# Optimization experiments

Measured on AMD Instinct MI355X. Metric: run time of the kernel, lower is better.

## Reference

```python
import jax, jax.numpy as jnp
import numpy as np
from jax import lax

N_LAYERS = 10  # Sinkhorn(n_layers=10)


def setup_inputs() -> dict:
    key = jax.random.key(0)
    k1, k2, k3 = jax.random.split(key, 3)
    S, NA, NB = 4, 4096, 4096
    alpha = jax.random.uniform(k1, (S, NA), jnp.float32, 0.05, 1.0)
    alpha = alpha / alpha.sum(-1, keepdims=True)  # probability simplex
    beta = jax.random.uniform(k2, (S, NB), jnp.float32, 0.05, 1.0)
    beta = beta / beta.sum(-1, keepdims=True)
    C = jax.random.uniform(k3, (NA, NB), jnp.float32)  # nonneg cost matrix
    eps = jnp.float32(0.1)  # entropic regularization
    return {"alpha": alpha, "beta": beta, "C": C, "eps": eps}


def reference(alpha, beta, C, eps):
    # Log-domain Sinkhorn: f,g are dual potentials, shapes (S,NA)/(S,NB).
    log_alpha = jnp.log(alpha)
    log_beta = jnp.log(beta)

    def log_dot_exp(A, b):
        # A: (n, m), b: (S, m) -> (S, n); matches torch log_dot_exp (2D case)
        return jax.scipy.special.logsumexp((-A[None, :, :] + b[:, None, :]) / eps, axis=-1)

    def step(carry, _):
        _, g = carry
        f = eps * (log_alpha - log_dot_exp(C, g))
        g = eps * (log_beta - log_dot_exp(C.T, f))
        return (f, g), None

    f0 = jnp.zeros_like(alpha)
    g0 = jnp.zeros_like(beta)
    (f, g), _ = lax.scan(step, (f0, g0), None, length=N_LAYERS)
    return f, g
```

## Files before the change

### kernel.cpp

```cpp
#include <hip/hip_runtime.h>
#include <stdint.h>

#define NN 4096
#define NITER 10
#define ROWS 16
#define NBLK 256
#define THREADS 512

#define STG_OFF  131072
#define RED_OFF  148480

typedef float v2f __attribute__((ext_vector_type(2)));

static __device__ __forceinline__ unsigned short f2bf(float f) {
  union { float f; unsigned int i; } x; x.f = f;
  unsigned int i = x.i;
  i += 0x7FFFu + ((i >> 16) & 1u);
  return (unsigned short)(i >> 16);
}
static __device__ __forceinline__ unsigned int pk2(float a, float b) {
  return (unsigned int)f2bf(a) | ((unsigned int)f2bf(b) << 16);
}
static __device__ __forceinline__ float2 unpk(unsigned int u) {
  union { unsigned int i; float f; } a, b;
  a.i = u << 16; b.i = u & 0xFFFF0000u;
  return make_float2(a.f, b.f);
}
static __device__ __forceinline__ float read_eps(const void* p) {
  float f = *(const float*)p;
  if (f > 1e-4f && f < 1.0f) return f;
  union { unsigned int i; float f; } x;
  x.i = ((unsigned int)*(const unsigned short*)p) << 16;
  return x.f;
}
static __device__ __forceinline__ void astore8(unsigned long long* p, unsigned long long v) {
  __hip_atomic_store(p, v, __ATOMIC_RELAXED, __HIP_MEMORY_SCOPE_AGENT);
}
static __device__ __forceinline__ float4 up4(unsigned int w0, unsigned int w1) {
  float2 a = unpk(w0), b = unpk(w1);
  return make_float4(a.x, a.y, b.x, b.y);
}
static __device__ __forceinline__ v2f mk2(float a, float b) {
  v2f r; r.x = a; r.y = b; return r;
}
#define FMA2(a, b, c) __builtin_elementwise_fma(a, b, c)

__global__ __launch_bounds__(256) void zero_flags(unsigned int* __restrict__ c) {
#pragma unroll
  for (int k = 0; k < 32; ++k) c[threadIdx.x + k * 256] = 0;
}

static __device__ __forceinline__ void wait_group(
    const unsigned int* flags, int q, unsigned token) {
  const unsigned int* p = flags + (q * 64 + (threadIdx.x & 63)) * 16;
  for (;;) {
    unsigned v = __hip_atomic_load(p, __ATOMIC_RELAXED,
                                   __HIP_MEMORY_SCOPE_AGENT);
    if (__ballot(v >= token) == 0xFFFFFFFFFFFFFFFFull) break;
    __builtin_amdgcn_s_sleep(1);
  }
}

__global__ __launch_bounds__(THREADS, 1) void sinkhorn_all(
    const float* __restrict__ alpha, const float* __restrict__ beta,
    const float* __restrict__ C, const void* __restrict__ epsp,
    unsigned short* __restrict__ K, unsigned long long* __restrict__ u_ep,
    unsigned long long* __restrict__ v_ep, unsigned int* __restrict__ u_flags,
    unsigned int* __restrict__ v_flags, float* __restrict__ out) {
  __shared__ float4 smem4[9792];
  char* sm = (char*)smem4;
  const int t = threadIdx.x, b = blockIdx.x;
  const int wave = t >> 6, lane = t & 63;
  const int own = ((b & 7) << 5) | (b >> 3);
  const int base0 = own * ROWS;
  const float eps = read_eps(epsp);
  const float nie = -1.0f / eps;

#pragma unroll 2
  for (int r = 0; r < ROWS; ++r) {
    const float4* Crow = (const float4*)(C + (size_t)(base0 + r) * NN) + t * 2;
    float4 c0 = Crow[0], c1 = Crow[1];
    uint4 k0;
    k0.x = pk2(__expf(c0.x * nie), __expf(c0.y * nie));
    k0.y = pk2(__expf(c0.z * nie), __expf(c0.w * nie));
    k0.z = pk2(__expf(c1.x * nie), __expf(c1.y * nie));
    k0.w = pk2(__expf(c1.z * nie), __expf(c1.w * nie));
    ((uint4*)(K + (size_t)(base0 + r) * NN))[t] = k0;
  }

  {
    const int p = t & 3, cb = p * 4, rb = t >> 2;
#pragma unroll 1
    for (int q2 = 0; q2 < 32; q2 += 8) {
      float4 cv[8];
#pragma unroll
      for (int z = 0; z < 8; ++z)
        cv[z] = *(const float4*)(C + (size_t)((q2 + z) * 128 + rb) * NN + base0 + cb);
#pragma unroll
      for (int z = 0; z < 8; ++z) {
        int n = (q2 + z) * 128 + rb;
        int u16 = ((n >> 10) * 8 + ((n >> 3) & 7)) * 256 + ((n >> 6) & 15) * 16;
        int jo = (n & 7) * 2;
        *(unsigned short*)(sm + (size_t)(u16 + cb + 0) * 16 + jo) = f2bf(__expf(cv[z].x * nie));
        *(unsigned short*)(sm + (size_t)(u16 + cb + 1) * 16 + jo) = f2bf(__expf(cv[z].y * nie));
        *(unsigned short*)(sm + (size_t)(u16 + cb + 2) * 16 + jo) = f2bf(__expf(cv[z].z * nie));
        *(unsigned short*)(sm + (size_t)(u16 + cb + 3) * 16 + jo) = f2bf(__expf(cv[z].w * nie));
      }
    }
  }
  __syncthreads();

  for (int it = 0; it < NITER; ++it) {
    v2f acc01[2] = {}, acc23[2] = {};
    const int r0 = base0 + wave * 2;
    const uint4* Kr0 = (const uint4*)(K + (size_t)r0 * NN);
    const uint4* VB = (const uint4*)(v_ep + (size_t)(it - 1) * NN);
#pragma unroll 1
    for (int q = 0; q < 4; ++q) {
      if (it > 0) wait_group(v_flags, q, (unsigned)it);
      {
        float4* L = (float4*)(sm + STG_OFF);
        int s0 = t * 2;
        float4 f0, f1;
        if (it == 0) {
          f0 = f1 = make_float4(1.f, 1.f, 1.f, 1.f);
        } else {
          uint4 sv = VB[q * 512 + t];
          f0 = up4(sv.x, sv.y);
          f1 = up4(sv.z, sv.w);
        }
        L[((s0 & 7) * 128) + (s0 >> 3)] = f0;
        L[(((s0 + 1) & 7) * 128) + ((s0 + 1) >> 3)] = f1;
      }
      __syncthreads();
      uint4 karr[4];
#pragma unroll
      for (int ms = 0; ms < 2; ++ms) {
        int moff = q * 128 + ms * 64 + lane;
        karr[ms * 2 + 0] = Kr0[moff];
        karr[ms * 2 + 1] = Kr0[moff + 512];
      }
      const float4* VL = (const float4*)(sm + STG_OFF);
#pragma unroll
      for (int ms = 0; ms < 2; ++ms) {
        int lb = ms * 64 + lane;
        float4 vv[8];
#pragma unroll
        for (int j = 0; j < 8; ++j) vv[j] = VL[j * 128 + lb];
#pragma unroll
        for (int rr = 0; rr < 2; ++rr) {
          unsigned int cw[4] = {karr[ms*2+rr].x, karr[ms*2+rr].y,
                                karr[ms*2+rr].z, karr[ms*2+rr].w};
#pragma unroll
          for (int w = 0; w < 4; ++w) {
            float2 f = unpk(cw[w]);
            float4 va = vv[2 * w], vb = vv[2 * w + 1];
            acc01[rr] = FMA2(mk2(f.x, f.x), mk2(va.x, va.y), acc01[rr]);
            acc23[rr] = FMA2(mk2(f.x, f.x), mk2(va.z, va.w), acc23[rr]);
            acc01[rr] = FMA2(mk2(f.y, f.y), mk2(vb.x, vb.y), acc01[rr]);
            acc23[rr] = FMA2(mk2(f.y, f.y), mk2(vb.z, vb.w), acc23[rr]);
          }
        }
      }
      __syncthreads();
    }
    float accf[2][4];
#pragma unroll
    for (int rr = 0; rr < 2; ++rr) {
      accf[rr][0] = acc01[rr].x; accf[rr][1] = acc01[rr].y;
      accf[rr][2] = acc23[rr].x; accf[rr][3] = acc23[rr].y;
    }
#pragma unroll
    for (int off = 32; off > 0; off >>= 1)
#pragma unroll
      for (int rr = 0; rr < 2; ++rr)
#pragma unroll
        for (int s = 0; s < 4; ++s)
          accf[rr][s] += __shfl_xor(accf[rr][s], off);
    if (lane < 2) {
      int row = r0 + lane;
      float ux = alpha[0 * NN + row] / accf[lane][0];
      float uy = alpha[1 * NN + row] / accf[lane][1];
      float uz = alpha[2 * NN + row] / accf[lane][2];
      float uw = alpha[3 * NN + row] / accf[lane][3];
      unsigned long long ub = (unsigned long long)pk2(ux, uy) |
                              ((unsigned long long)pk2(uz, uw) << 32);
      astore8(u_ep + (size_t)it * NN + row, ub);
      if (it == NITER - 1) {
        out[0 * NN + row] = eps * __logf(ux);
        out[1 * NN + row] = eps * __logf(uy);
        out[2 * NN + row] = eps * __logf(uz);
        out[3 * NN + row] = eps * __logf(uw);
      }
    }
    __syncthreads();
    if (t == 0)
      __hip_atomic_store(u_flags + own * 16, (unsigned)(it + 1),
                         __ATOMIC_RELAXED, __HIP_MEMORY_SCOPE_AGENT);

    v2f bacc01 = {}, bacc23 = {};
    const int c = t & 15, k2 = (t >> 4) & 15, half = t >> 8;
    const uint4* UB = (const uint4*)(u_ep + (size_t)it * NN);
#pragma unroll 1
    for (int q = 0; q < 4; ++q) {
      wait_group(u_flags, q, (unsigned)(it + 1));
      {
        char* US = sm + STG_OFF;
        uint4 su = UB[q * 512 + t];
        float4 f0 = up4(su.x, su.y), f1 = up4(su.z, su.w);
        int n0 = t * 2;
        *(float4*)(US + (n0 + 0) * 16 + ((n0 + 0) >> 4) * 16) = f0;
        *(float4*)(US + (n0 + 1) * 16 + ((n0 + 1) >> 4) * 16) = f1;
      }
      __syncthreads();
      const char* US = sm + STG_OFF;
#pragma unroll
      for (int i = 0; i < 4; ++i) {
        uint4 kt = ((const uint4*)sm)[(q * 8 + half * 4 + i) * 256 + k2 * 16 + c];
        int nb = k2 * 64 + (half * 4 + i) * 8;
        unsigned int kw[4] = {kt.x, kt.y, kt.z, kt.w};
#pragma unroll
        for (int w = 0; w < 4; ++w) {
          float2 f = unpk(kw[w]);
          int j0 = nb + 2 * w, j1 = nb + 2 * w + 1;
          float4 u0 = *(const float4*)(US + j0 * 16 + (j0 >> 4) * 16);
          float4 u1 = *(const float4*)(US + j1 * 16 + (j1 >> 4) * 16);
          bacc01 = FMA2(mk2(f.x, f.x), mk2(u0.x, u0.y), bacc01);
          bacc23 = FMA2(mk2(f.x, f.x), mk2(u0.z, u0.w), bacc23);
          bacc01 = FMA2(mk2(f.y, f.y), mk2(u1.x, u1.y), bacc01);
          bacc23 = FMA2(mk2(f.y, f.y), mk2(u1.z, u1.w), bacc23);
        }
      }
      __syncthreads();
    }
    {
      float4* red = (float4*)(sm + RED_OFF);
      red[(half * 16 + k2) * 16 + c] =
          make_float4(bacc01.x, bacc01.y, bacc23.x, bacc23.y);
    }
    __syncthreads();
    if (t < 16) {
      const float4* red = (const float4*)(sm + RED_OFF);
      float4 a = make_float4(0.f, 0.f, 0.f, 0.f);
#pragma unroll
      for (int g = 0; g < 32; ++g) {
        float4 r = red[g * 16 + t];
        a.x += r.x; a.y += r.y; a.z += r.z; a.w += r.w;
      }
      int m = base0 + t;
      float vx = beta[0 * NN + m] / a.x;
      float vy = beta[1 * NN + m] / a.y;
      float vz = beta[2 * NN + m] / a.z;
      float vw = beta[3 * NN + m] / a.w;
      unsigned long long vb = (unsigned long long)pk2(vx, vy) |
                              ((unsigned long long)pk2(vz, vw) << 32);
      astore8(v_ep + (size_t)it * NN + m, vb);
      if (it == NITER - 1) {
        out[4 * NN + 0 * NN + m] = eps * __logf(vx);
        out[4 * NN + 1 * NN + m] = eps * __logf(vy);
        out[4 * NN + 2 * NN + m] = eps * __logf(vz);
        out[4 * NN + 3 * NN + m] = eps * __logf(vw);
      }
    }
    __syncthreads();
    if (t == 0 && it < NITER - 1)
      __hip_atomic_store(v_flags + own * 16, (unsigned)(it + 1),
                         __ATOMIC_RELAXED, __HIP_MEMORY_SCOPE_AGENT);
  }
}

extern "C" void kernel_launch(void* const* d_in, const int* in_sizes, int n_in,
                              void* d_out, int out_size, void* d_ws, size_t ws_size,
                              hipStream_t stream) {
  (void)in_sizes; (void)n_in; (void)out_size; (void)ws_size;
  const float* alpha = (const float*)d_in[0];
  const float* beta  = (const float*)d_in[1];
  const float* C     = (const float*)d_in[2];
  const void*  epsp  = d_in[3];

  char* ws = (char*)d_ws;
  unsigned short* K        = (unsigned short*)ws;
  unsigned long long* u_ep = (unsigned long long*)(ws + 33554432);
  unsigned long long* v_ep = (unsigned long long*)(ws + 33554432 + 327680);
  unsigned int* u_flags    = (unsigned int*)(ws + 33554432 + 655360);
  unsigned int* v_flags    = (unsigned int*)(ws + 33554432 + 655360 + 16384);
  float* out = (float*)d_out;

  zero_flags<<<1, 256, 0, stream>>>(u_flags);
  sinkhorn_all<<<NBLK, THREADS, 0, stream>>>(alpha, beta, C, epsp, K,
                                             u_ep, v_ep, u_flags, v_flags, out);
}
```

Measured before the change: 269.6 us.

## Double block size to 1024 threads, one row per wave, prefetch K before barrier

Raises the block from 512 to 1024 threads and repartitions every phase: the K precompute, the transposed LDS fill, the u-update (now one row per wave instead of two) and the v-update (half the k-chunks per thread). The K loads from global and LDS are issued before the staging barrier so they overlap the wait. The v-reduction now does an in-wave shuffle over the k2 groups before the LDS write, shrinking the cross-wave reduction. This adds latency hiding through more waves per CU, but barrier cost grows with 16 waves and half the threads sit idle during staging.

```diff
diff --git a/kernel.cpp b/kernel.cpp
--- a/kernel.cpp
+++ b/kernel.cpp
@@ -5,7 +5,7 @@
 #define NITER 10
 #define ROWS 16
 #define NBLK 256
-#define THREADS 512
+#define THREADS 1024
 
 #define STG_OFF  131072
 #define RED_OFF  148480
@@ -67,7 +67,7 @@
     unsigned short* __restrict__ K, unsigned long long* __restrict__ u_ep,
     unsigned long long* __restrict__ v_ep, unsigned int* __restrict__ u_flags,
     unsigned int* __restrict__ v_flags, float* __restrict__ out) {
-  __shared__ float4 smem4[9792];
+  __shared__ float4 smem4[9536];
   char* sm = (char*)smem4;
   const int t = threadIdx.x, b = blockIdx.x;
   const int wave = t >> 6, lane = t & 63;
@@ -77,28 +77,29 @@
   const float nie = -1.0f / eps;
 
 #pragma unroll 2
-  for (int r = 0; r < ROWS; ++r) {
-    const float4* Crow = (const float4*)(C + (size_t)(base0 + r) * NN) + t * 2;
+  for (int rp = 0; rp < 8; ++rp) {
+    const int r = rp * 2 + (t >> 9);
+    const float4* Crow = (const float4*)(C + (size_t)(base0 + r) * NN) + (t & 511) * 2;
     float4 c0 = Crow[0], c1 = Crow[1];
     uint4 k0;
     k0.x = pk2(__expf(c0.x * nie), __expf(c0.y * nie));
     k0.y = pk2(__expf(c0.z * nie), __expf(c0.w * nie));
     k0.z = pk2(__expf(c1.x * nie), __expf(c1.y * nie));
     k0.w = pk2(__expf(c1.z * nie), __expf(c1.w * nie));
-    ((uint4*)(K + (size_t)(base0 + r) * NN))[t] = k0;
+    ((uint4*)(K + (size_t)(base0 + r) * NN))[t & 511] = k0;
   }
 
   {
     const int p = t & 3, cb = p * 4, rb = t >> 2;
 #pragma unroll 1
-    for (int q2 = 0; q2 < 32; q2 += 8) {
+    for (int q2 = 0; q2 < 16; q2 += 8) {
       float4 cv[8];
 #pragma unroll
       for (int z = 0; z < 8; ++z)
-        cv[z] = *(const float4*)(C + (size_t)((q2 + z) * 128 + rb) * NN + base0 + cb);
+        cv[z] = *(const float4*)(C + (size_t)((q2 + z) * 256 + rb) * NN + base0 + cb);
 #pragma unroll
       for (int z = 0; z < 8; ++z) {
-        int n = (q2 + z) * 128 + rb;
+        int n = (q2 + z) * 256 + rb;
         int u16 = ((n >> 10) * 8 + ((n >> 3) & 7)) * 256 + ((n >> 6) & 15) * 16;
         int jo = (n & 7) * 2;
         *(unsigned short*)(sm + (size_t)(u16 + cb + 0) * 16 + jo) = f2bf(__expf(cv[z].x * nie));
@@ -111,14 +112,17 @@
   __syncthreads();
 
   for (int it = 0; it < NITER; ++it) {
-    v2f acc01[2] = {}, acc23[2] = {};
-    const int r0 = base0 + wave * 2;
+    v2f acc01 = {}, acc23 = {};
+    const int r0 = base0 + wave;
     const uint4* Kr0 = (const uint4*)(K + (size_t)r0 * NN);
     const uint4* VB = (const uint4*)(v_ep + (size_t)(it - 1) * NN);
 #pragma unroll 1
     for (int q = 0; q < 4; ++q) {
       if (it > 0) wait_group(v_flags, q, (unsigned)it);
-      {
+      uint4 karr[2];
+      karr[0] = Kr0[q * 128 + lane];
+      karr[1] = Kr0[q * 128 + 64 + lane];
+      if (t < 512) {
         float4* L = (float4*)(sm + STG_OFF);
         int s0 = t * 2;
         float4 f0, f1;
@@ -133,13 +137,6 @@
         L[(((s0 + 1) & 7) * 128) + ((s0 + 1) >> 3)] = f1;
       }
       __syncthreads();
-      uint4 karr[4];
-#pragma unroll
-      for (int ms = 0; ms < 2; ++ms) {
-        int moff = q * 128 + ms * 64 + lane;
-        karr[ms * 2 + 0] = Kr0[moff];
-        karr[ms * 2 + 1] = Kr0[moff + 512];
-      }
       const float4* VL = (const float4*)(sm + STG_OFF);
 #pragma unroll
       for (int ms = 0; ms < 2; ++ms) {
@@ -147,50 +144,41 @@
         float4 vv[8];
 #pragma unroll
         for (int j = 0; j < 8; ++j) vv[j] = VL[j * 128 + lb];
-#pragma unroll
-        for (int rr = 0; rr < 2; ++rr) {
-          unsigned int cw[4] = {karr[ms*2+rr].x, karr[ms*2+rr].y,
-                                karr[ms*2+rr].z, karr[ms*2+rr].w};
-#pragma unroll
-          for (int w = 0; w < 4; ++w) {
-            float2 f = unpk(cw[w]);
-            float4 va = vv[2 * w], vb = vv[2 * w + 1];
-            acc01[rr] = FMA2(mk2(f.x, f.x), mk2(va.x, va.y), acc01[rr]);
-            acc23[rr] = FMA2(mk2(f.x, f.x), mk2(va.z, va.w), acc23[rr]);
-            acc01[rr] = FMA2(mk2(f.y, f.y), mk2(vb.x, vb.y), acc01[rr]);
-            acc23[rr] = FMA2(mk2(f.y, f.y), mk2(vb.z, vb.w), acc23[rr]);
-          }
-        }
-      }
-      __syncthreads();
-    }
-    float accf[2][4];
-#pragma unroll
-    for (int rr = 0; rr < 2; ++rr) {
-      accf[rr][0] = acc01[rr].x; accf[rr][1] = acc01[rr].y;
-      accf[rr][2] = acc23[rr].x; accf[rr][3] = acc23[rr].y;
-    }
-#pragma unroll
-    for (int off = 32; off > 0; off >>= 1)
-#pragma unroll
-      for (int rr = 0; rr < 2; ++rr)
+        unsigned int cw[4] = {karr[ms].x, karr[ms].y, karr[ms].z, karr[ms].w};
+#pragma unroll
+        for (int w = 0; w < 4; ++w) {
+          float2 f = unpk(cw[w]);
+          float4 va = vv[2 * w], vb = vv[2 * w + 1];
+          acc01 = FMA2(mk2(f.x, f.x), mk2(va.x, va.y), acc01);
+          acc23 = FMA2(mk2(f.x, f.x), mk2(va.z, va.w), acc23);
+          acc01 = FMA2(mk2(f.y, f.y), mk2(vb.x, vb.y), acc01);
+          acc23 = FMA2(mk2(f.y, f.y), mk2(vb.z, vb.w), acc23);
+        }
+      }
+      __syncthreads();
+    }
+    {
+      float accf[4] = {acc01.x, acc01.y, acc23.x, acc23.y};
+#pragma unroll
+      for (int off = 32; off > 0; off >>= 1)
 #pragma unroll
         for (int s = 0; s < 4; ++s)
-          accf[rr][s] += __shfl_xor(accf[rr][s], off);
-    if (lane < 2) {
-      int row = r0 + lane;
-      float ux = alpha[0 * NN + row] / accf[lane][0];
-      float uy = alpha[1 * NN + row] / accf[lane][1];
-      float uz = alpha[2 * NN + row] / accf[lane][2];
-      float uw = alpha[3 * NN + row] / accf[lane][3];
-      unsigned long long ub = (unsigned long long)pk2(ux, uy) |
-                              ((unsigned long long)pk2(uz, uw) << 32);
-      astore8(u_ep + (size_t)it * NN + row, ub);
-      if (it == NITER - 1) {
-        out[0 * NN + row] = eps * __logf(ux);
-        out[1 * NN + row] = eps * __logf(uy);
-        out[2 * NN + row] = eps * __logf(uz);
-        out[3 * NN + row] = eps * __logf(uw);
+          accf[s] += __shfl_xor(accf[s], off);
+      if (lane == 0) {
+        int row = r0;
+        float ux = alpha[0 * NN + row] / accf[0];
+        float uy = alpha[1 * NN + row] / accf[1];
+        float uz = alpha[2 * NN + row] / accf[2];
+        float uw = alpha[3 * NN + row] / accf[3];
+        unsigned long long ub = (unsigned long long)pk2(ux, uy) |
+                                ((unsigned long long)pk2(uz, uw) << 32);
+        astore8(u_ep + (size_t)it * NN + row, ub);
+        if (it == NITER - 1) {
+          out[0 * NN + row] = eps * __logf(ux);
+          out[1 * NN + row] = eps * __logf(uy);
+          out[2 * NN + row] = eps * __logf(uz);
+          out[3 * NN + row] = eps * __logf(uw);
+        }
       }
     }
     __syncthreads();
@@ -204,7 +192,11 @@
 #pragma unroll 1
     for (int q = 0; q < 4; ++q) {
       wait_group(u_flags, q, (unsigned)(it + 1));
-      {
+      uint4 kt[2];
+#pragma unroll
+      for (int i = 0; i < 2; ++i)
+        kt[i] = ((const uint4*)sm)[(q * 8 + half * 2 + i) * 256 + k2 * 16 + c];
+      if (t < 512) {
         char* US = sm + STG_OFF;
         uint4 su = UB[q * 512 + t];
         float4 f0 = up4(su.x, su.y), f1 = up4(su.z, su.w);
@@ -215,10 +207,9 @@
       __syncthreads();
       const char* US = sm + STG_OFF;
 #pragma unroll
-      for (int i = 0; i < 4; ++i) {
-        uint4 kt = ((const uint4*)sm)[(q * 8 + half * 4 + i) * 256 + k2 * 16 + c];
-        int nb = k2 * 64 + (half * 4 + i) * 8;
-        unsigned int kw[4] = {kt.x, kt.y, kt.z, kt.w};
+      for (int i = 0; i < 2; ++i) {
+        int nb = k2 * 64 + (half * 2 + i) * 8;
+        unsigned int kw[4] = {kt[i].x, kt[i].y, kt[i].z, kt[i].w};
 #pragma unroll
         for (int w = 0; w < 4; ++w) {
           float2 f = unpk(kw[w]);
@@ -234,16 +225,23 @@
       __syncthreads();
     }
     {
-      float4* red = (float4*)(sm + RED_OFF);
-      red[(half * 16 + k2) * 16 + c] =
-          make_float4(bacc01.x, bacc01.y, bacc23.x, bacc23.y);
+      float bf[4] = {bacc01.x, bacc01.y, bacc23.x, bacc23.y};
+#pragma unroll
+      for (int s = 0; s < 4; ++s) {
+        bf[s] += __shfl_xor(bf[s], 16);
+        bf[s] += __shfl_xor(bf[s], 32);
+      }
+      if (lane < 16) {
+        float4* red = (float4*)(sm + RED_OFF);
+        red[wave * 16 + lane] = make_float4(bf[0], bf[1], bf[2], bf[3]);
+      }
     }
     __syncthreads();
     if (t < 16) {
       const float4* red = (const float4*)(sm + RED_OFF);
       float4 a = make_float4(0.f, 0.f, 0.f, 0.f);
 #pragma unroll
-      for (int g = 0; g < 32; ++g) {
+      for (int g = 0; g < 16; ++g) {
         float4 r = red[g * 16 + t];
         a.x += r.x; a.y += r.y; a.z += r.z; a.w += r.w;
       }
```

New measurement: 287.4 us. +6.6%, slower.

## Double-buffer staging with single upfront flag wait and swizzled bf16 LDS vectors

Applied to the files above, without the earlier changes.

Both matvec phases now wait once for all producer flags up front, replacing the four per-quarter waits. Each quarter double-buffers the staged vector in LDS while prefetching the next quarter's K tile into registers. Vectors stay bf16 in LDS under an XOR swizzle, which halves staging bytes and drops one barrier per quarter. The column pass is remapped so each thread handles two columns, and a wave shuffle reduction replaces most of the LDS reduction. The single wait gives up overlap between early quarters and late producers, and the bounded spin can exit before the data is ready.

```diff
diff --git a/kernel.cpp b/kernel.cpp
--- a/kernel.cpp
+++ b/kernel.cpp
@@ -8,7 +8,8 @@
 #define THREADS 512
 
 #define STG_OFF  131072
-#define RED_OFF  148480
+#define RED_OFF  147456
+#define SWZ(s) ((((unsigned)(s)) * 16u) ^ ((((unsigned)(s)) >> 3 & 7u) << 4))
 
 typedef float v2f __attribute__((ext_vector_type(2)));
 
@@ -36,10 +37,6 @@
 static __device__ __forceinline__ void astore8(unsigned long long* p, unsigned long long v) {
   __hip_atomic_store(p, v, __ATOMIC_RELAXED, __HIP_MEMORY_SCOPE_AGENT);
 }
-static __device__ __forceinline__ float4 up4(unsigned int w0, unsigned int w1) {
-  float2 a = unpk(w0), b = unpk(w1);
-  return make_float4(a.x, a.y, b.x, b.y);
-}
 static __device__ __forceinline__ v2f mk2(float a, float b) {
   v2f r; r.x = a; r.y = b; return r;
 }
@@ -50,13 +47,16 @@
   for (int k = 0; k < 32; ++k) c[threadIdx.x + k * 256] = 0;
 }
 
-static __device__ __forceinline__ void wait_group(
-    const unsigned int* flags, int q, unsigned token) {
-  const unsigned int* p = flags + (q * 64 + (threadIdx.x & 63)) * 16;
-  for (;;) {
-    unsigned v = __hip_atomic_load(p, __ATOMIC_RELAXED,
-                                   __HIP_MEMORY_SCOPE_AGENT);
-    if (__ballot(v >= token) == 0xFFFFFFFFFFFFFFFFull) break;
+static __device__ __forceinline__ void wait_all(
+    const unsigned int* flags, unsigned token) {
+  const unsigned int* p = flags + (threadIdx.x & 63) * 16;
+  for (int spin = 0; spin < 200000; ++spin) {
+    unsigned a = __hip_atomic_load(p, __ATOMIC_RELAXED, __HIP_MEMORY_SCOPE_AGENT);
+    unsigned b = __hip_atomic_load(p + 64 * 16, __ATOMIC_RELAXED, __HIP_MEMORY_SCOPE_AGENT);
+    unsigned c = __hip_atomic_load(p + 128 * 16, __ATOMIC_RELAXED, __HIP_MEMORY_SCOPE_AGENT);
+    unsigned d = __hip_atomic_load(p + 192 * 16, __ATOMIC_RELAXED, __HIP_MEMORY_SCOPE_AGENT);
+    unsigned mn = min(min(a, b), min(c, d));
+    if (__ballot(mn >= token) == 0xFFFFFFFFFFFFFFFFull) break;
     __builtin_amdgcn_s_sleep(1);
   }
 }
@@ -67,7 +67,7 @@
     unsigned short* __restrict__ K, unsigned long long* __restrict__ u_ep,
     unsigned long long* __restrict__ v_ep, unsigned int* __restrict__ u_flags,
     unsigned int* __restrict__ v_flags, float* __restrict__ out) {
-  __shared__ float4 smem4[9792];
+  __shared__ float4 smem4[9344];
   char* sm = (char*)smem4;
   const int t = threadIdx.x, b = blockIdx.x;
   const int wave = t >> 6, lane = t & 63;
@@ -110,87 +110,101 @@
   }
   __syncthreads();
 
+  const uint4 ONES = make_uint4(0x3F803F80u, 0x3F803F80u, 0x3F803F80u, 0x3F803F80u);
+
   for (int it = 0; it < NITER; ++it) {
     v2f acc01[2] = {}, acc23[2] = {};
     const int r0 = base0 + wave * 2;
     const uint4* Kr0 = (const uint4*)(K + (size_t)r0 * NN);
     const uint4* VB = (const uint4*)(v_ep + (size_t)(it - 1) * NN);
+    if (it > 0) wait_all(v_flags, (unsigned)it);
+    {
+      uint4 sv = (it == 0) ? ONES : VB[t];
+      *(uint4*)(sm + STG_OFF + SWZ((t & 3) * 128 + (t >> 2))) = sv;
+    }
+    uint4 ka[4];
+#pragma unroll
+    for (int ms = 0; ms < 2; ++ms) {
+      ka[ms * 2 + 0] = Kr0[ms * 64 + lane];
+      ka[ms * 2 + 1] = Kr0[512 + ms * 64 + lane];
+    }
+    __syncthreads();
 #pragma unroll 1
     for (int q = 0; q < 4; ++q) {
-      if (it > 0) wait_group(v_flags, q, (unsigned)it);
-      {
-        float4* L = (float4*)(sm + STG_OFF);
-        int s0 = t * 2;
-        float4 f0, f1;
-        if (it == 0) {
-          f0 = f1 = make_float4(1.f, 1.f, 1.f, 1.f);
-        } else {
-          uint4 sv = VB[q * 512 + t];
-          f0 = up4(sv.x, sv.y);
-          f1 = up4(sv.z, sv.w);
-        }
-        L[((s0 & 7) * 128) + (s0 >> 3)] = f0;
-        L[(((s0 + 1) & 7) * 128) + ((s0 + 1) >> 3)] = f1;
-      }
-      __syncthreads();
-      uint4 karr[4];
+      uint4 sv_n, ka_n[4];
+      if (q < 3) {
+        sv_n = (it == 0) ? ONES : VB[(q + 1) * 512 + t];
+#pragma unroll
+        for (int ms = 0; ms < 2; ++ms) {
+          ka_n[ms * 2 + 0] = Kr0[(q + 1) * 128 + ms * 64 + lane];
+          ka_n[ms * 2 + 1] = Kr0[512 + (q + 1) * 128 + ms * 64 + lane];
+        }
+      }
+      const char* stg = sm + STG_OFF + (q & 1) * 8192;
 #pragma unroll
       for (int ms = 0; ms < 2; ++ms) {
-        int moff = q * 128 + ms * 64 + lane;
-        karr[ms * 2 + 0] = Kr0[moff];
-        karr[ms * 2 + 1] = Kr0[moff + 512];
-      }
-      const float4* VL = (const float4*)(sm + STG_OFF);
-#pragma unroll
-      for (int ms = 0; ms < 2; ++ms) {
-        int lb = ms * 64 + lane;
-        float4 vv[8];
-#pragma unroll
-        for (int j = 0; j < 8; ++j) vv[j] = VL[j * 128 + lb];
+        const int lb = ms * 64 + lane;
+        uint4 vq[4];
+#pragma unroll
+        for (int jj = 0; jj < 4; ++jj)
+          vq[jj] = *(const uint4*)(stg + SWZ(jj * 128 + lb));
+        float2 va01[4], va23[4], vb01[4], vb23[4];
+#pragma unroll
+        for (int w = 0; w < 4; ++w) {
+          va01[w] = unpk(vq[w].x); va23[w] = unpk(vq[w].y);
+          vb01[w] = unpk(vq[w].z); vb23[w] = unpk(vq[w].w);
+        }
 #pragma unroll
         for (int rr = 0; rr < 2; ++rr) {
-          unsigned int cw[4] = {karr[ms*2+rr].x, karr[ms*2+rr].y,
-                                karr[ms*2+rr].z, karr[ms*2+rr].w};
+          unsigned int cw[4] = {ka[ms * 2 + rr].x, ka[ms * 2 + rr].y,
+                                ka[ms * 2 + rr].z, ka[ms * 2 + rr].w};
 #pragma unroll
           for (int w = 0; w < 4; ++w) {
             float2 f = unpk(cw[w]);
-            float4 va = vv[2 * w], vb = vv[2 * w + 1];
-            acc01[rr] = FMA2(mk2(f.x, f.x), mk2(va.x, va.y), acc01[rr]);
-            acc23[rr] = FMA2(mk2(f.x, f.x), mk2(va.z, va.w), acc23[rr]);
-            acc01[rr] = FMA2(mk2(f.y, f.y), mk2(vb.x, vb.y), acc01[rr]);
-            acc23[rr] = FMA2(mk2(f.y, f.y), mk2(vb.z, vb.w), acc23[rr]);
+            acc01[rr] = FMA2(mk2(f.x, f.x), mk2(va01[w].x, va01[w].y), acc01[rr]);
+            acc23[rr] = FMA2(mk2(f.x, f.x), mk2(va23[w].x, va23[w].y), acc23[rr]);
+            acc01[rr] = FMA2(mk2(f.y, f.y), mk2(vb01[w].x, vb01[w].y), acc01[rr]);
+            acc23[rr] = FMA2(mk2(f.y, f.y), mk2(vb23[w].x, vb23[w].y), acc23[rr]);
           }
         }
       }
+      if (q < 3) {
+        *(uint4*)(sm + STG_OFF + ((q + 1) & 1) * 8192 +
+                  SWZ((t & 3) * 128 + (t >> 2))) = sv_n;
+#pragma unroll
+        for (int z = 0; z < 4; ++z) ka[z] = ka_n[z];
+      }
       __syncthreads();
     }
-    float accf[2][4];
-#pragma unroll
-    for (int rr = 0; rr < 2; ++rr) {
-      accf[rr][0] = acc01[rr].x; accf[rr][1] = acc01[rr].y;
-      accf[rr][2] = acc23[rr].x; accf[rr][3] = acc23[rr].y;
-    }
-#pragma unroll
-    for (int off = 32; off > 0; off >>= 1)
-#pragma unroll
-      for (int rr = 0; rr < 2; ++rr)
-#pragma unroll
-        for (int s = 0; s < 4; ++s)
-          accf[rr][s] += __shfl_xor(accf[rr][s], off);
-    if (lane < 2) {
-      int row = r0 + lane;
-      float ux = alpha[0 * NN + row] / accf[lane][0];
-      float uy = alpha[1 * NN + row] / accf[lane][1];
-      float uz = alpha[2 * NN + row] / accf[lane][2];
-      float uw = alpha[3 * NN + row] / accf[lane][3];
-      unsigned long long ub = (unsigned long long)pk2(ux, uy) |
-                              ((unsigned long long)pk2(uz, uw) << 32);
-      astore8(u_ep + (size_t)it * NN + row, ub);
-      if (it == NITER - 1) {
-        out[0 * NN + row] = eps * __logf(ux);
-        out[1 * NN + row] = eps * __logf(uy);
-        out[2 * NN + row] = eps * __logf(uz);
-        out[3 * NN + row] = eps * __logf(uw);
+    {
+      float accf[2][4];
+#pragma unroll
+      for (int rr = 0; rr < 2; ++rr) {
+        accf[rr][0] = acc01[rr].x; accf[rr][1] = acc01[rr].y;
+        accf[rr][2] = acc23[rr].x; accf[rr][3] = acc23[rr].y;
+      }
+#pragma unroll
+      for (int off = 32; off > 0; off >>= 1)
+#pragma unroll
+        for (int rr = 0; rr < 2; ++rr)
+#pragma unroll
+          for (int s = 0; s < 4; ++s)
+            accf[rr][s] += __shfl_xor(accf[rr][s], off);
+      if (lane < 2) {
+        int row = r0 + lane;
+        float ux = alpha[0 * NN + row] / accf[lane][0];
+        float uy = alpha[1 * NN + row] / accf[lane][1];
+        float uz = alpha[2 * NN + row] / accf[lane][2];
+        float uw = alpha[3 * NN + row] / accf[lane][3];
+        unsigned long long ub = (unsigned long long)pk2(ux, uy) |
+                                ((unsigned long long)pk2(uz, uw) << 32);
+        astore8(u_ep + (size_t)it * NN + row, ub);
+        if (it == NITER - 1) {
+          out[0 * NN + row] = eps * __logf(ux);
+          out[1 * NN + row] = eps * __logf(uy);
+          out[2 * NN + row] = eps * __logf(uz);
+          out[3 * NN + row] = eps * __logf(uw);
+        }
       }
     }
     __syncthreads();
@@ -198,53 +212,94 @@
       __hip_atomic_store(u_flags + own * 16, (unsigned)(it + 1),
                          __ATOMIC_RELAXED, __HIP_MEMORY_SCOPE_AGENT);
 
-    v2f bacc01 = {}, bacc23 = {};
-    const int c = t & 15, k2 = (t >> 4) & 15, half = t >> 8;
+    v2f bacc01[2] = {}, bacc23[2] = {};
+    const int c = t & 7, k2 = (t >> 3) & 15, half = t >> 7;
     const uint4* UB = (const uint4*)(u_ep + (size_t)it * NN);
+    wait_all(u_flags, (unsigned)(it + 1));
+    {
+      uint4 su = UB[t];
+      *(uint4*)(sm + STG_OFF + SWZ((t & 3) * 128 + (t >> 2))) = su;
+    }
+    uint4 kt[4];
+#pragma unroll
+    for (int i = 0; i < 2; ++i) {
+      int s = half * 2 + i;
+      kt[i * 2 + 0] = ((const uint4*)sm)[(0 * 8 + s) * 256 + k2 * 16 + c];
+      kt[i * 2 + 1] = ((const uint4*)sm)[(0 * 8 + s) * 256 + k2 * 16 + c + 8];
+    }
+    __syncthreads();
 #pragma unroll 1
     for (int q = 0; q < 4; ++q) {
-      wait_group(u_flags, q, (unsigned)(it + 1));
-      {
-        char* US = sm + STG_OFF;
-        uint4 su = UB[q * 512 + t];
-        float4 f0 = up4(su.x, su.y), f1 = up4(su.z, su.w);
-        int n0 = t * 2;
-        *(float4*)(US + (n0 + 0) * 16 + ((n0 + 0) >> 4) * 16) = f0;
-        *(float4*)(US + (n0 + 1) * 16 + ((n0 + 1) >> 4) * 16) = f1;
+      uint4 su_n, kt_n[4];
+      if (q < 3) {
+        su_n = UB[(q + 1) * 512 + t];
+#pragma unroll
+        for (int i = 0; i < 2; ++i) {
+          int s = half * 2 + i;
+          kt_n[i * 2 + 0] = ((const uint4*)sm)[((q + 1) * 8 + s) * 256 + k2 * 16 + c];
+          kt_n[i * 2 + 1] = ((const uint4*)sm)[((q + 1) * 8 + s) * 256 + k2 * 16 + c + 8];
+        }
+      }
+      const char* stg = sm + STG_OFF + (q & 1) * 8192;
+#pragma unroll
+      for (int i = 0; i < 2; ++i) {
+        const int s = half * 2 + i;
+        uint4 uq[4];
+#pragma unroll
+        for (int jj = 0; jj < 4; ++jj)
+          uq[jj] = *(const uint4*)(stg + SWZ(jj * 128 + k2 * 8 + s));
+        float2 u01[8], u23[8];
+#pragma unroll
+        for (int jj = 0; jj < 4; ++jj) {
+          u01[2 * jj]     = unpk(uq[jj].x); u23[2 * jj]     = unpk(uq[jj].y);
+          u01[2 * jj + 1] = unpk(uq[jj].z); u23[2 * jj + 1] = unpk(uq[jj].w);
+        }
+#pragma unroll
+        for (int cs = 0; cs < 2; ++cs) {
+          unsigned int kw[4] = {kt[i * 2 + cs].x, kt[i * 2 + cs].y,
+                                kt[i * 2 + cs].z, kt[i * 2 + cs].w};
+#pragma unroll
+          for (int w = 0; w < 4; ++w) {
+            float2 f = unpk(kw[w]);
+            bacc01[cs] = FMA2(mk2(f.x, f.x), mk2(u01[2 * w].x, u01[2 * w].y), bacc01[cs]);
+            bacc23[cs] = FMA2(mk2(f.x, f.x), mk2(u23[2 * w].x, u23[2 * w].y), bacc23[cs]);
+            bacc01[cs] = FMA2(mk2(f.y, f.y), mk2(u01[2 * w + 1].x, u01[2 * w + 1].y), bacc01[cs]);
+            bacc23[cs] = FMA2(mk2(f.y, f.y), mk2(u23[2 * w + 1].x, u23[2 * w + 1].y), bacc23[cs]);
+          }
+        }
+      }
+      if (q < 3) {
+        *(uint4*)(sm + STG_OFF + ((q + 1) & 1) * 8192 +
+                  SWZ((t & 3) * 128 + (t >> 2))) = su_n;
+#pragma unroll
+        for (int z = 0; z < 4; ++z) kt[z] = kt_n[z];
       }
       __syncthreads();
-      const char* US = sm + STG_OFF;
-#pragma unroll
-      for (int i = 0; i < 4; ++i) {
-        uint4 kt = ((const uint4*)sm)[(q * 8 + half * 4 + i) * 256 + k2 * 16 + c];
-        int nb = k2 * 64 + (half * 4 + i) * 8;
-        unsigned int kw[4] = {kt.x, kt.y, kt.z, kt.w};
-#pragma unroll
-        for (int w = 0; w < 4; ++w) {
-          float2 f = unpk(kw[w]);
-          int j0 = nb + 2 * w, j1 = nb + 2 * w + 1;
-          float4 u0 = *(const float4*)(US + j0 * 16 + (j0 >> 4) * 16);
-          float4 u1 = *(const float4*)(US + j1 * 16 + (j1 >> 4) * 16);
-          bacc01 = FMA2(mk2(f.x, f.x), mk2(u0.x, u0.y), bacc01);
-          bacc23 = FMA2(mk2(f.x, f.x), mk2(u0.z, u0.w), bacc23);
-          bacc01 = FMA2(mk2(f.y, f.y), mk2(u1.x, u1.y), bacc01);
-          bacc23 = FMA2(mk2(f.y, f.y), mk2(u1.z, u1.w), bacc23);
-        }
-      }
-      __syncthreads();
     }
     {
-      float4* red = (float4*)(sm + RED_OFF);
-      red[(half * 16 + k2) * 16 + c] =
-          make_float4(bacc01.x, bacc01.y, bacc23.x, bacc23.y);
+      float bf0[4] = {bacc01[0].x, bacc01[0].y, bacc23[0].x, bacc23[0].y};
+      float bf1[4] = {bacc01[1].x, bacc01[1].y, bacc23[1].x, bacc23[1].y};
+#pragma unroll
+      for (int off = 8; off <= 32; off <<= 1)
+#pragma unroll
+        for (int s2 = 0; s2 < 4; ++s2) {
+          bf0[s2] += __shfl_xor(bf0[s2], off);
+          bf1[s2] += __shfl_xor(bf1[s2], off);
+        }
+      if (lane < 8) {
+        float4* red = (float4*)(sm + RED_OFF);
+        red[(wave * 8 + lane) * 2 + 0] = make_float4(bf0[0], bf0[1], bf0[2], bf0[3]);
+        red[(wave * 8 + lane) * 2 + 1] = make_float4(bf1[0], bf1[1], bf1[2], bf1[3]);
+      }
     }
     __syncthreads();
     if (t < 16) {
       const float4* red = (const float4*)(sm + RED_OFF);
+      const int cc = t & 7, sel = t >> 3;
       float4 a = make_float4(0.f, 0.f, 0.f, 0.f);
 #pragma unroll
-      for (int g = 0; g < 32; ++g) {
-        float4 r = red[g * 16 + t];
+      for (int g = 0; g < 8; ++g) {
+        float4 r = red[(g * 8 + cc) * 2 + sel];
         a.x += r.x; a.y += r.y; a.z += r.z; a.w += r.w;
       }
       int m = base0 + t;
```

Result: slower. 286.8 us (+6.4%).

## Hold transposed K tile in registers and drop per-quarter staging syncs

Applied to the files above, without the earlier changes.

Each thread now loads its slice of the transposed bf16 K tile from LDS into registers once before the iteration loop, so the column pass (g update) reads only u from LDS, staged in full per half-wave group rather than quarter by quarter. The row pass places the v staging buffer directly in LDS with a new transposed layout and removes the second barrier per quarter. The cross-thread reduction now uses shuffles before a smaller LDS reduction. Register pressure rises sharply with 16 uint4 held per thread. The spin-wait gets an iteration cap, which silently gives up after timeout. Dropping a barrier around LDS buffer reuse risks a race between quarters.

```diff
diff --git a/kernel.cpp b/kernel.cpp
--- a/kernel.cpp
+++ b/kernel.cpp
@@ -7,8 +7,9 @@
 #define NBLK 256
 #define THREADS 512
 
-#define STG_OFF  131072
-#define RED_OFF  148480
+#define RED_OFF 67584
+#define TRS(col) (((((col) & 7) * 512) + ((col) >> 3)) * 16)
+#define LIN(k) ((k) * 16 + ((((k) >> 5)) << 4))
 
 typedef float v2f __attribute__((ext_vector_type(2)));
 
@@ -53,7 +54,7 @@
 static __device__ __forceinline__ void wait_group(
     const unsigned int* flags, int q, unsigned token) {
   const unsigned int* p = flags + (q * 64 + (threadIdx.x & 63)) * 16;
-  for (;;) {
+  for (int spin = 0; spin < 400000; ++spin) {
     unsigned v = __hip_atomic_load(p, __ATOMIC_RELAXED,
                                    __HIP_MEMORY_SCOPE_AGENT);
     if (__ballot(v >= token) == 0xFFFFFFFFFFFFFFFFull) break;
@@ -67,7 +68,7 @@
     unsigned short* __restrict__ K, unsigned long long* __restrict__ u_ep,
     unsigned long long* __restrict__ v_ep, unsigned int* __restrict__ u_flags,
     unsigned int* __restrict__ v_flags, float* __restrict__ out) {
-  __shared__ float4 smem4[9792];
+  __shared__ float4 smem4[8192];
   char* sm = (char*)smem4;
   const int t = threadIdx.x, b = blockIdx.x;
   const int wave = t >> 6, lane = t & 63;
@@ -110,6 +111,18 @@
   }
   __syncthreads();
 
+  const int cB = t & 7, k2n = (t >> 3) & 15, hB = t >> 7;
+  const int kbase = hB * 1024 + k2n * 64;
+  uint4 ktr[16];
+#pragma unroll
+  for (int s = 0; s < 8; ++s) {
+    ktr[s]     = ((const uint4*)sm)[(hB * 8 + s) * 256 + k2n * 16 + cB];
+    ktr[s + 8] = ((const uint4*)sm)[(hB * 8 + s) * 256 + k2n * 16 + cB + 8];
+  }
+  __syncthreads();
+
+  const uint4 ONES = make_uint4(0x3F803F80u, 0x3F803F80u, 0x3F803F80u, 0x3F803F80u);
+
   for (int it = 0; it < NITER; ++it) {
     v2f acc01[2] = {}, acc23[2] = {};
     const int r0 = base0 + wave * 2;
@@ -118,79 +131,69 @@
 #pragma unroll 1
     for (int q = 0; q < 4; ++q) {
       if (it > 0) wait_group(v_flags, q, (unsigned)it);
+      uint4 ka[4];
+      ka[0] = Kr0[(q * 2) * 64 + lane];
+      ka[1] = Kr0[512 + (q * 2) * 64 + lane];
+      ka[2] = Kr0[(q * 2 + 1) * 64 + lane];
+      ka[3] = Kr0[512 + (q * 2 + 1) * 64 + lane];
       {
-        float4* L = (float4*)(sm + STG_OFF);
-        int s0 = t * 2;
-        float4 f0, f1;
-        if (it == 0) {
-          f0 = f1 = make_float4(1.f, 1.f, 1.f, 1.f);
-        } else {
-          uint4 sv = VB[q * 512 + t];
-          f0 = up4(sv.x, sv.y);
-          f1 = up4(sv.z, sv.w);
-        }
-        L[((s0 & 7) * 128) + (s0 >> 3)] = f0;
-        L[(((s0 + 1) & 7) * 128) + ((s0 + 1) >> 3)] = f1;
+        uint4 sv = (it == 0) ? ONES : VB[q * 512 + t];
+        const int col0 = q * 1024 + t * 2;
+        *(float4*)(sm + TRS(col0))     = up4(sv.x, sv.y);
+        *(float4*)(sm + TRS(col0 + 1)) = up4(sv.z, sv.w);
       }
       __syncthreads();
-      uint4 karr[4];
-#pragma unroll
-      for (int ms = 0; ms < 2; ++ms) {
-        int moff = q * 128 + ms * 64 + lane;
-        karr[ms * 2 + 0] = Kr0[moff];
-        karr[ms * 2 + 1] = Kr0[moff + 512];
-      }
-      const float4* VL = (const float4*)(sm + STG_OFF);
-#pragma unroll
-      for (int ms = 0; ms < 2; ++ms) {
-        int lb = ms * 64 + lane;
+#pragma unroll
+      for (int ii = 0; ii < 2; ++ii) {
+        const int i = q * 2 + ii;
         float4 vv[8];
 #pragma unroll
-        for (int j = 0; j < 8; ++j) vv[j] = VL[j * 128 + lb];
+        for (int j = 0; j < 8; ++j)
+          vv[j] = *(const float4*)(sm + (j * 512 + i * 64 + lane) * 16);
 #pragma unroll
         for (int rr = 0; rr < 2; ++rr) {
-          unsigned int cw[4] = {karr[ms*2+rr].x, karr[ms*2+rr].y,
-                                karr[ms*2+rr].z, karr[ms*2+rr].w};
+          const uint4 kk = ka[ii * 2 + rr];
+          unsigned cw[4] = {kk.x, kk.y, kk.z, kk.w};
 #pragma unroll
           for (int w = 0; w < 4; ++w) {
             float2 f = unpk(cw[w]);
-            float4 va = vv[2 * w], vb = vv[2 * w + 1];
-            acc01[rr] = FMA2(mk2(f.x, f.x), mk2(va.x, va.y), acc01[rr]);
-            acc23[rr] = FMA2(mk2(f.x, f.x), mk2(va.z, va.w), acc23[rr]);
-            acc01[rr] = FMA2(mk2(f.y, f.y), mk2(vb.x, vb.y), acc01[rr]);
-            acc23[rr] = FMA2(mk2(f.y, f.y), mk2(vb.z, vb.w), acc23[rr]);
+            acc01[rr] = FMA2(mk2(f.x, f.x), mk2(vv[2*w].x, vv[2*w].y), acc01[rr]);
+            acc23[rr] = FMA2(mk2(f.x, f.x), mk2(vv[2*w].z, vv[2*w].w), acc23[rr]);
+            acc01[rr] = FMA2(mk2(f.y, f.y), mk2(vv[2*w+1].x, vv[2*w+1].y), acc01[rr]);
+            acc23[rr] = FMA2(mk2(f.y, f.y), mk2(vv[2*w+1].z, vv[2*w+1].w), acc23[rr]);
           }
         }
       }
-      __syncthreads();
-    }
-    float accf[2][4];
-#pragma unroll
-    for (int rr = 0; rr < 2; ++rr) {
-      accf[rr][0] = acc01[rr].x; accf[rr][1] = acc01[rr].y;
-      accf[rr][2] = acc23[rr].x; accf[rr][3] = acc23[rr].y;
-    }
-#pragma unroll
-    for (int off = 32; off > 0; off >>= 1)
-#pragma unroll
-      for (int rr = 0; rr < 2; ++rr)
-#pragma unroll
-        for (int s = 0; s < 4; ++s)
-          accf[rr][s] += __shfl_xor(accf[rr][s], off);
-    if (lane < 2) {
-      int row = r0 + lane;
-      float ux = alpha[0 * NN + row] / accf[lane][0];
-      float uy = alpha[1 * NN + row] / accf[lane][1];
-      float uz = alpha[2 * NN + row] / accf[lane][2];
-      float uw = alpha[3 * NN + row] / accf[lane][3];
-      unsigned long long ub = (unsigned long long)pk2(ux, uy) |
-                              ((unsigned long long)pk2(uz, uw) << 32);
-      astore8(u_ep + (size_t)it * NN + row, ub);
-      if (it == NITER - 1) {
-        out[0 * NN + row] = eps * __logf(ux);
-        out[1 * NN + row] = eps * __logf(uy);
-        out[2 * NN + row] = eps * __logf(uz);
-        out[3 * NN + row] = eps * __logf(uw);
+    }
+    {
+      float accf[2][4];
+#pragma unroll
+      for (int rr = 0; rr < 2; ++rr) {
+        accf[rr][0] = acc01[rr].x; accf[rr][1] = acc01[rr].y;
+        accf[rr][2] = acc23[rr].x; accf[rr][3] = acc23[rr].y;
+      }
+#pragma unroll
+      for (int off = 32; off > 0; off >>= 1)
+#pragma unroll
+        for (int rr = 0; rr < 2; ++rr)
+#pragma unroll
+          for (int s = 0; s < 4; ++s)
+            accf[rr][s] += __shfl_xor(accf[rr][s], off);
+      if (lane < 2) {
+        int row = r0 + lane;
+        float ux = alpha[0 * NN + row] / accf[lane][0];
+        float uy = alpha[1 * NN + row] / accf[lane][1];
+        float uz = alpha[2 * NN + row] / accf[lane][2];
+        float uw = alpha[3 * NN + row] / accf[lane][3];
+        unsigned long long ub = (unsigned long long)pk2(ux, uy) |
+                                ((unsigned long long)pk2(uz, uw) << 32);
+        astore8(u_ep + (size_t)it * NN + row, ub);
+        if (it == NITER - 1) {
+          out[0 * NN + row] = eps * __logf(ux);
+          out[1 * NN + row] = eps * __logf(uy);
+          out[2 * NN + row] = eps * __logf(uz);
+          out[3 * NN + row] = eps * __logf(uw);
+        }
       }
     }
     __syncthreads();
@@ -198,53 +201,64 @@
       __hip_atomic_store(u_flags + own * 16, (unsigned)(it + 1),
                          __ATOMIC_RELAXED, __HIP_MEMORY_SCOPE_AGENT);
 
-    v2f bacc01 = {}, bacc23 = {};
-    const int c = t & 15, k2 = (t >> 4) & 15, half = t >> 8;
+    v2f bacc01[2] = {}, bacc23[2] = {};
     const uint4* UB = (const uint4*)(u_ep + (size_t)it * NN);
-#pragma unroll 1
-    for (int q = 0; q < 4; ++q) {
-      wait_group(u_flags, q, (unsigned)(it + 1));
-      {
-        char* US = sm + STG_OFF;
-        uint4 su = UB[q * 512 + t];
-        float4 f0 = up4(su.x, su.y), f1 = up4(su.z, su.w);
-        int n0 = t * 2;
-        *(float4*)(US + (n0 + 0) * 16 + ((n0 + 0) >> 4) * 16) = f0;
-        *(float4*)(US + (n0 + 1) * 16 + ((n0 + 1) >> 4) * 16) = f1;
-      }
-      __syncthreads();
-      const char* US = sm + STG_OFF;
-#pragma unroll
-      for (int i = 0; i < 4; ++i) {
-        uint4 kt = ((const uint4*)sm)[(q * 8 + half * 4 + i) * 256 + k2 * 16 + c];
-        int nb = k2 * 64 + (half * 4 + i) * 8;
-        unsigned int kw[4] = {kt.x, kt.y, kt.z, kt.w};
-#pragma unroll
-        for (int w = 0; w < 4; ++w) {
-          float2 f = unpk(kw[w]);
-          int j0 = nb + 2 * w, j1 = nb + 2 * w + 1;
-          float4 u0 = *(const float4*)(US + j0 * 16 + (j0 >> 4) * 16);
-          float4 u1 = *(const float4*)(US + j1 * 16 + (j1 >> 4) * 16);
-          bacc01 = FMA2(mk2(f.x, f.x), mk2(u0.x, u0.y), bacc01);
-          bacc23 = FMA2(mk2(f.x, f.x), mk2(u0.z, u0.w), bacc23);
-          bacc01 = FMA2(mk2(f.y, f.y), mk2(u1.x, u1.y), bacc01);
-          bacc23 = FMA2(mk2(f.y, f.y), mk2(u1.z, u1.w), bacc23);
+    wait_group(u_flags, hB, (unsigned)(it + 1));
+    {
+      uint4 su[8];
+#pragma unroll
+      for (int z = 0; z < 8; ++z) su[z] = UB[hB * 512 + lane * 8 + z];
+#pragma unroll
+      for (int z = 0; z < 8; ++z) {
+        const int k0 = hB * 1024 + lane * 16 + 2 * z;
+        *(float4*)(sm + LIN(k0))     = up4(su[z].x, su[z].y);
+        *(float4*)(sm + LIN(k0 + 1)) = up4(su[z].z, su[z].w);
+      }
+    }
+#pragma unroll
+    for (int s = 0; s < 8; ++s) {
+      unsigned cw0[4] = {ktr[s].x, ktr[s].y, ktr[s].z, ktr[s].w};
+      unsigned cw1[4] = {ktr[s + 8].x, ktr[s + 8].y, ktr[s + 8].z, ktr[s + 8].w};
+#pragma unroll
+      for (int w = 0; w < 4; ++w) {
+        const int k = kbase + s * 8 + 2 * w;
+        float4 u0 = *(const float4*)(sm + LIN(k));
+        float4 u1 = *(const float4*)(sm + LIN(k + 1));
+        float2 f0 = unpk(cw0[w]), f1 = unpk(cw1[w]);
+        bacc01[0] = FMA2(mk2(f0.x, f0.x), mk2(u0.x, u0.y), bacc01[0]);
+        bacc23[0] = FMA2(mk2(f0.x, f0.x), mk2(u0.z, u0.w), bacc23[0]);
+        bacc01[0] = FMA2(mk2(f0.y, f0.y), mk2(u1.x, u1.y), bacc01[0]);
+        bacc23[0] = FMA2(mk2(f0.y, f0.y), mk2(u1.z, u1.w), bacc23[0]);
+        bacc01[1] = FMA2(mk2(f1.x, f1.x), mk2(u0.x, u0.y), bacc01[1]);
+        bacc23[1] = FMA2(mk2(f1.x, f1.x), mk2(u0.z, u0.w), bacc23[1]);
+        bacc01[1] = FMA2(mk2(f1.y, f1.y), mk2(u1.x, u1.y), bacc01[1]);
+        bacc23[1] = FMA2(mk2(f1.y, f1.y), mk2(u1.z, u1.w), bacc23[1]);
+      }
+    }
+    {
+      float bf0[4] = {bacc01[0].x, bacc01[0].y, bacc23[0].x, bacc23[0].y};
+      float bf1[4] = {bacc01[1].x, bacc01[1].y, bacc23[1].x, bacc23[1].y};
+#pragma unroll
+      for (int off = 8; off <= 32; off <<= 1)
+#pragma unroll
+        for (int s2 = 0; s2 < 4; ++s2) {
+          bf0[s2] += __shfl_xor(bf0[s2], off);
+          bf1[s2] += __shfl_xor(bf1[s2], off);
         }
-      }
-      __syncthreads();
-    }
-    {
-      float4* red = (float4*)(sm + RED_OFF);
-      red[(half * 16 + k2) * 16 + c] =
-          make_float4(bacc01.x, bacc01.y, bacc23.x, bacc23.y);
+      if (lane < 8) {
+        float4* red = (float4*)(sm + RED_OFF);
+        red[(wave * 8 + lane) * 2 + 0] = make_float4(bf0[0], bf0[1], bf0[2], bf0[3]);
+        red[(wave * 8 + lane) * 2 + 1] = make_float4(bf1[0], bf1[1], bf1[2], bf1[3]);
+      }
     }
     __syncthreads();
     if (t < 16) {
       const float4* red = (const float4*)(sm + RED_OFF);
+      const int cc = t & 7, sel = t >> 3;
       float4 a = make_float4(0.f, 0.f, 0.f, 0.f);
 #pragma unroll
-      for (int g = 0; g < 32; ++g) {
-        float4 r = red[g * 16 + t];
+      for (int g = 0; g < 8; ++g) {
+        float4 r = red[(g * 8 + cc) * 2 + sel];
         a.x += r.x; a.y += r.y; a.z += r.z; a.w += r.w;
       }
       int m = base0 + t;
```

Result: slower. 460.1 us (+70.7%).
